# Kernel optimization log

Measured on AMD Instinct MI355X. Metric: run time of the kernel, lower is better.

The kernel has to match this reference:

```python
import jax, jax.numpy as jnp
import numpy as np

N = 100000      # nodes
E = 1600000     # edges
D_IN, H1, H2, D_OUT = 128, 64, 64, 64


def setup_inputs() -> dict:
    key = jax.random.key(0)
    ks = jax.random.split(key, 9)
    x = jax.random.normal(ks[0], (N, D_IN), dtype=jnp.float32)
    edge_index = jax.random.randint(ks[1], (2, E), 0, N, dtype=jnp.int32)
    def lin(k, fan_in, fan_out):
        s = 1.0 / np.sqrt(fan_in)
        return jax.random.uniform(k, (fan_in, fan_out), jnp.float32, -s, s)
    W1 = lin(ks[2], D_IN, H1); b1 = jnp.zeros((H1,), jnp.float32)
    W2 = lin(ks[3], H1, H2);  b2 = jnp.zeros((H2,), jnp.float32)
    W3 = lin(ks[4], H2, D_OUT); b3 = jnp.zeros((D_OUT,), jnp.float32)
    return {"x": x, "W1": W1, "b1": b1, "W2": W2, "b2": b2,
            "W3": W3, "b3": b3, "edge_index": edge_index}


def reference(x, W1, b1, W2, b2, W3, b3, edge_index):
    src, dst = edge_index[0], edge_index[1]
    # GCN symmetric normalization with self-loops: deg = in-degree + 1
    deg = jnp.zeros((N,), x.dtype).at[dst].add(1.0) + 1.0
    dinv = jax.lax.rsqrt(deg)                 # [N]
    norm = dinv[src] * dinv[dst]              # [E] edge weights
    self_norm = dinv * dinv                   # [N] self-loop weights

    def conv(h, W, b):
        h = h @ W                             # transform first (PyG GCNConv)
        msg = h[src] * norm[:, None]          # [E, F] gathered messages
        agg = jnp.zeros_like(h).at[dst].add(msg) + self_norm[:, None] * h
        return agg + b

    h = jax.nn.relu(conv(x, W1, b1))          # dropout is identity in eval
    h = jax.nn.relu(conv(h, W2, b2))
    return conv(h, W3, b3)
```

## Files before the change

kernel.cpp:

```cpp
#include <hip/hip_runtime.h>
#include <hip/hip_bf16.h>

#define D_IN 128
#define F 64
#define R_EDGES 4096

__global__ __launch_bounds__(256) void part1_kernel(
        const int* __restrict__ src, const int* __restrict__ dst, int E,
        unsigned long long M37, int cap1, uint2* __restrict__ ebufB,
        int* __restrict__ bcur1) {
    __shared__ int wcnt[64], incl64[64], cur[64], gbase[16];
    const int t = threadIdx.x, w = t >> 6, lane = t & 63;
    const int base = blockIdx.x * R_EDGES;
    const int lim = min(base + R_EDGES, E);

    if (t < 64) wcnt[t] = 0;
    __syncthreads();

    for (int i = base + t; i < lim; i += 256) {
        int d = dst[i];
        int b = (int)(((unsigned long long)(unsigned)d * M37) >> 37) >> 4;
        atomicAdd(&wcnt[b * 4 + w], 1);
    }
    __syncthreads();

    if (t < 64) {
        int v = wcnt[t], x = v;
        for (int dlt = 1; dlt < 64; dlt <<= 1) { int y = __shfl_up(x, dlt); if (lane >= dlt) x += y; }
        incl64[t] = x;
        wcnt[t] = x - v;
    }
    __syncthreads();
    if (t < 16) {
        int T = incl64[t * 4 + 3] - (t ? incl64[t * 4 - 1] : 0);
        gbase[t] = T > 0 ? atomicAdd(&bcur1[t], T) : 0;
    }
    __syncthreads();
    if (t < 64) cur[t] = gbase[t >> 2] + wcnt[t] - wcnt[(t >> 2) << 2];
    __syncthreads();

    for (int i = base + t; i < lim; i += 256) {
        int s = src[i], d = dst[i];
        int b = (int)(((unsigned long long)(unsigned)d * M37) >> 37) >> 4;
        int p = atomicAdd(&cur[b * 4 + w], 1);
        ebufB[(size_t)b * cap1 + p] = make_uint2((unsigned)s, (unsigned)d);
    }
}

#define BPB2 27
__global__ __launch_bounds__(256) void part2_kernel(
        const uint2* __restrict__ ebufB, const int* __restrict__ bcur1,
        unsigned long long M37, int cap1, int cap2,
        uint2* __restrict__ ebufA, int* __restrict__ bcur2) {
    __shared__ int wcnt[64], incl64[64], cur[64], gbase[16];
    const int t = threadIdx.x, w = t >> 6, lane = t & 63;
    const int b1 = blockIdx.x / BPB2, r = blockIdx.x % BPB2;
    const int cnt1 = bcur1[b1];
    const int beg = r * R_EDGES, lim = min(beg + R_EDGES, cnt1);
    if (beg >= cnt1) return;
    const uint2* in = ebufB + (size_t)b1 * cap1;

    if (t < 64) wcnt[t] = 0;
    __syncthreads();

    for (int i = beg + t; i < lim; i += 256) {
        unsigned d = in[i].y;
        int b = (int)(((unsigned long long)d * M37) >> 37) & 15;
        atomicAdd(&wcnt[b * 4 + w], 1);
    }
    __syncthreads();

    if (t < 64) {
        int v = wcnt[t], x = v;
        for (int dlt = 1; dlt < 64; dlt <<= 1) { int y = __shfl_up(x, dlt); if (lane >= dlt) x += y; }
        incl64[t] = x;
        wcnt[t] = x - v;
    }
    __syncthreads();
    if (t < 16) {
        int T = incl64[t * 4 + 3] - (t ? incl64[t * 4 - 1] : 0);
        gbase[t] = T > 0 ? atomicAdd(&bcur2[b1 * 16 + t], T) : 0;
    }
    __syncthreads();
    if (t < 64) cur[t] = gbase[t >> 2] + wcnt[t] - wcnt[(t >> 2) << 2];
    __syncthreads();

    for (int i = beg + t; i < lim; i += 256) {
        uint2 e = in[i];
        int b = (int)(((unsigned long long)e.y * M37) >> 37) & 15;
        int p = atomicAdd(&cur[b * 4 + w], 1);
        ebufA[(size_t)(b1 * 16 + b) * cap2 + p] = e;
    }
}

__global__ __launch_bounds__(256) void scan256_kernel(const int* __restrict__ bcur2,
                                                      int* __restrict__ bbase,
                                                      int* __restrict__ offsets, int n, int E) {
    __shared__ int tmp[256];
    int t = threadIdx.x;
    int v = bcur2[t];
    tmp[t] = v;
    __syncthreads();
    for (int off = 1; off < 256; off <<= 1) {
        int a = (t >= off) ? tmp[t - off] : 0;
        __syncthreads();
        if (t >= off) tmp[t] += a;
        __syncthreads();
    }
    bbase[t] = tmp[t] - v;
    if (t == 0) offsets[n] = E;
}

__global__ __launch_bounds__(256) void bsort_kernel(
        const uint2* __restrict__ ebufA, const int* __restrict__ bcur2,
        const int* __restrict__ bbase, int cap2, int NPB, int n,
        int* __restrict__ csr, int* __restrict__ offsets, float* __restrict__ dinv) {
    __shared__ int cnt[512], excl[512];
    const int sb = blockIdx.x, t = threadIdx.x;
    const int node0 = sb * NPB;
    const int nn = min(NPB, n - node0);
    if (nn <= 0) return;
    const int cE = bcur2[sb];
    const int base = bbase[sb];
    const uint2* eb = ebufA + (size_t)sb * cap2;

    for (int i = t; i < 512; i += 256) cnt[i] = 0;
    __syncthreads();
    for (int i = t; i < cE; i += 256) atomicAdd(&cnt[eb[i].y - node0], 1);
    __syncthreads();

    if (t < 64) {
        int carry = 0;
        for (int c = 0; c < 8; ++c) {
            int v = cnt[c * 64 + t], x = v;
            for (int dlt = 1; dlt < 64; dlt <<= 1) { int y = __shfl_up(x, dlt); if (t >= dlt) x += y; }
            excl[c * 64 + t] = carry + x - v;
            carry += __shfl(x, 63);
        }
    }
    __syncthreads();

    for (int i = t; i < nn; i += 256) {
        offsets[node0 + i] = base + excl[i];
        dinv[node0 + i] = rsqrtf((float)cnt[i] + 1.0f);
    }
    __syncthreads();
    for (int i = t; i < 512; i += 256) cnt[i] = excl[i];
    __syncthreads();
    for (int i = t; i < cE; i += 256) {
        uint2 e = eb[i];
        int p = atomicAdd(&cnt[e.y - node0], 1);
        csr[base + p] = (int)e.x;
    }
}

template<int K, bool RELU_IN>
__global__ __launch_bounds__(256) void gemm_kernel(
        const float* __restrict__ A, const float* __restrict__ W,
        const float* __restrict__ dinv, float* __restrict__ h2, int n) {
    constexpr int F4 = K / 4;
    __shared__ float4 Al[64 * F4];
    __shared__ float  Wl[K * F];
    const int t = threadIdx.x;

    for (int i = t; i < K * F / 4; i += 256)
        ((float4*)Wl)[i] = ((const float4*)W)[i];

    const int row0 = blockIdx.x * 64;
    for (int i = t; i < 64 * F4; i += 256) {
        int r = i / F4, k4 = i % F4;
        int gr = row0 + r; if (gr >= n) gr = n - 1;
        float4 v = ((const float4*)(A + (size_t)gr * K))[k4];
        if (RELU_IN) {
            v.x = fmaxf(v.x, 0.f); v.y = fmaxf(v.y, 0.f);
            v.z = fmaxf(v.z, 0.f); v.w = fmaxf(v.w, 0.f);
        }
        Al[r * F4 + (k4 ^ ((r >> 2) & 7))] = v;
    }
    __syncthreads();

    const int rg = t >> 4, cg = t & 15;
    const int r0 = rg * 4, c0 = cg * 4;
    const int sw = rg & 7;

    float acc[4][4] = {};
#pragma unroll 2
    for (int k4 = 0; k4 < F4; ++k4) {
        float4 a[4];
#pragma unroll
        for (int i = 0; i < 4; ++i) a[i] = Al[(r0 + i) * F4 + (k4 ^ sw)];
#pragma unroll
        for (int j = 0; j < 4; ++j) {
            float4 w = *(const float4*)&Wl[(k4 * 4 + j) * F + c0];
#pragma unroll
            for (int i = 0; i < 4; ++i) {
                float av = (j == 0) ? a[i].x : (j == 1) ? a[i].y : (j == 2) ? a[i].z : a[i].w;
                acc[i][0] = fmaf(av, w.x, acc[i][0]);
                acc[i][1] = fmaf(av, w.y, acc[i][1]);
                acc[i][2] = fmaf(av, w.z, acc[i][2]);
                acc[i][3] = fmaf(av, w.w, acc[i][3]);
            }
        }
    }

#pragma unroll
    for (int i = 0; i < 4; ++i) {
        int gr = row0 + r0 + i;
        if (gr < n) {
            float dv = dinv[gr];
            float4 o = make_float4(acc[i][0] * dv, acc[i][1] * dv,
                                   acc[i][2] * dv, acc[i][3] * dv);
            *(float4*)&h2[(size_t)gr * F + c0] = o;
        }
    }
}

__global__ __launch_bounds__(256) void agg_kernel(
        const int* __restrict__ offsets, const int* __restrict__ csr,
        const float* __restrict__ dinv, const float* __restrict__ h2,
        const float* __restrict__ bvec, float* __restrict__ out, int n) {
    const int wid  = (int)((blockIdx.x * 256u + threadIdx.x) >> 6);
    const int lane = threadIdx.x & 63;
    const int g = lane >> 4, q = lane & 15;
    if (wid >= n) return;

    const int beg = offsets[wid], end = offsets[wid + 1];

    float4 acc = make_float4(0.f, 0.f, 0.f, 0.f);
    if (g == 0) acc = *(const float4*)&h2[(size_t)wid * F + q * 4];

    int j = beg + g;
    for (; j + 4 < end; j += 8) {
        int s0 = csr[j], s1 = csr[j + 4];
        float4 v0 = *(const float4*)&h2[(size_t)s0 * F + q * 4];
        float4 v1 = *(const float4*)&h2[(size_t)s1 * F + q * 4];
        acc.x += v0.x + v1.x; acc.y += v0.y + v1.y;
        acc.z += v0.z + v1.z; acc.w += v0.w + v1.w;
    }
    if (j < end) {
        int s0 = csr[j];
        float4 v0 = *(const float4*)&h2[(size_t)s0 * F + q * 4];
        acc.x += v0.x; acc.y += v0.y; acc.z += v0.z; acc.w += v0.w;
    }

    acc.x += __shfl_xor(acc.x, 16); acc.y += __shfl_xor(acc.y, 16);
    acc.z += __shfl_xor(acc.z, 16); acc.w += __shfl_xor(acc.w, 16);
    acc.x += __shfl_xor(acc.x, 32); acc.y += __shfl_xor(acc.y, 32);
    acc.z += __shfl_xor(acc.z, 32); acc.w += __shfl_xor(acc.w, 32);

    if (g == 0) {
        float dv = dinv[wid];
        float4 bb = *(const float4*)&bvec[q * 4];
        float4 o = make_float4(fmaf(dv, acc.x, bb.x), fmaf(dv, acc.y, bb.y),
                               fmaf(dv, acc.z, bb.z), fmaf(dv, acc.w, bb.w));
        *(float4*)&out[(size_t)wid * F + q * 4] = o;
    }
}

extern "C" void kernel_launch(void* const* d_in, const int* in_sizes, int n_in,
                              void* d_out, int out_size, void* d_ws, size_t ws_size,
                              hipStream_t stream) {
    const float* x   = (const float*)d_in[0];
    const float* W1  = (const float*)d_in[1];
    const float* b1  = (const float*)d_in[2];
    const float* W2  = (const float*)d_in[3];
    const float* b2  = (const float*)d_in[4];
    const float* W3  = (const float*)d_in[5];
    const float* b3  = (const float*)d_in[6];
    const int*   ei  = (const int*)d_in[7];

    const int n = in_sizes[0] / D_IN;
    const int E = in_sizes[7] / 2;
    const int* src = ei;
    const int* dst = ei + E;

    const int NPB = (n + 255) >> 8;
    const unsigned long long M37 = ((1ull << 37) / (unsigned long long)NPB) + 1;
    const int cap1 = E / 16 + 4096;
    const int cap2 = 8192;

    char* p = (char*)d_ws;
    auto alloc = [&](size_t bytes) { char* q = p; p += (bytes + 255) & ~(size_t)255; return q; };
    int*   bcur1   = (int*)  alloc((16 + 256) * 4);
    int*   bcur2   = bcur1 + 16;
    int*   bbase   = (int*)  alloc(256 * 4);
    int*   offsets = (int*)  alloc((size_t)(n + 1) * 4);
    float* dinv    = (float*)alloc((size_t)n * 4);
    int*   csr     = (int*)  alloc((size_t)E * 4);
    float* h2      = (float*)alloc((size_t)n * F * 4);
    float* outA    = (float*)alloc((size_t)n * F * 4);
    float* outF    = (float*)d_out;

    uint2* ebufB = (uint2*)h2;
    uint2* ebufA = (uint2*)outA;

    const int p1Blocks = (E + R_EDGES - 1) / R_EDGES;
    const int gBlocks  = (n + 63) / 64;
    const int aBlocks  = (int)(((size_t)n * 64 + 255) / 256);

    hipMemsetAsync(bcur1, 0, (16 + 256) * 4, stream);
    part1_kernel <<<p1Blocks,  256, 0, stream>>>(src, dst, E, M37, cap1, ebufB, bcur1);
    part2_kernel <<<16 * BPB2, 256, 0, stream>>>(ebufB, bcur1, M37, cap1, cap2, ebufA, bcur2);
    scan256_kernel<<<1,        256, 0, stream>>>(bcur2, bbase, offsets, n, E);
    bsort_kernel <<<256,       256, 0, stream>>>(ebufA, bcur2, bbase, cap2, NPB, n,
                                                 csr, offsets, dinv);

    gemm_kernel<D_IN, false><<<gBlocks, 256, 0, stream>>>(x, W1, dinv, h2, n);
    agg_kernel<<<aBlocks, 256, 0, stream>>>(offsets, csr, dinv, h2, b1, outA, n);

    gemm_kernel<F, true><<<gBlocks, 256, 0, stream>>>(outA, W2, dinv, h2, n);
    agg_kernel<<<aBlocks, 256, 0, stream>>>(offsets, csr, dinv, h2, b2, outA, n);

    gemm_kernel<F, true><<<gBlocks, 256, 0, stream>>>(outA, W3, dinv, h2, n);
    agg_kernel<<<aBlocks, 256, 0, stream>>>(offsets, csr, dinv, h2, b3, outF, n);
}
```

Before: 314.9 us.

## Fuse aggregation with next layer's GEMM and unroll neighbor gathers by four

Adds an aggmm kernel that aggregates 64 nodes per block (bias plus ReLU), keeps the results in swizzled shared memory, and immediately multiplies them by the next layer's weights. This removes two GEMM launches and the write and re-read of the intermediate activations. The agg loop is also unrolled to four gathers in flight per lane group. The risk is lower parallelism: one wave now handles 16 nodes in sequence, so fewer waves are available to hide gather latency.

```diff
diff --git a/kernel.cpp b/kernel.cpp
--- a/kernel.cpp
+++ b/kernel.cpp
@@ -215,6 +215,101 @@
     }
 }
 
+__global__ __launch_bounds__(256) void aggmm_kernel(
+        const int* __restrict__ offsets, const int* __restrict__ csr,
+        const float* __restrict__ dinv, const float* __restrict__ hin,
+        const float* __restrict__ bvec, const float* __restrict__ W,
+        float* __restrict__ hout, int n) {
+    __shared__ float4 Al[64 * 16];
+    __shared__ float  Wl[64 * F];
+    const int t = threadIdx.x;
+
+    for (int i = t; i < 64 * F / 4; i += 256)
+        ((float4*)Wl)[i] = ((const float4*)W)[i];
+
+    const int row0 = blockIdx.x * 64;
+    const int wv = t >> 6, lane = t & 63;
+    const int g = lane >> 4, q = lane & 15;
+
+    for (int i = 0; i < 16; ++i) {
+        const int r = wv * 16 + i;
+        const int node = row0 + r;
+        if (node < n) {
+            float4 acc = make_float4(0.f, 0.f, 0.f, 0.f);
+            if (g == 0) acc = *(const float4*)&hin[(size_t)node * F + q * 4];
+            const int beg = offsets[node], end = offsets[node + 1];
+            int j = beg + g;
+            for (; j + 12 < end; j += 16) {
+                int s0 = csr[j], s1 = csr[j + 4], s2 = csr[j + 8], s3 = csr[j + 12];
+                float4 v0 = *(const float4*)&hin[(size_t)s0 * F + q * 4];
+                float4 v1 = *(const float4*)&hin[(size_t)s1 * F + q * 4];
+                float4 v2 = *(const float4*)&hin[(size_t)s2 * F + q * 4];
+                float4 v3 = *(const float4*)&hin[(size_t)s3 * F + q * 4];
+                acc.x += (v0.x + v1.x) + (v2.x + v3.x);
+                acc.y += (v0.y + v1.y) + (v2.y + v3.y);
+                acc.z += (v0.z + v1.z) + (v2.z + v3.z);
+                acc.w += (v0.w + v1.w) + (v2.w + v3.w);
+            }
+            for (; j < end; j += 4) {
+                int s0 = csr[j];
+                float4 v0 = *(const float4*)&hin[(size_t)s0 * F + q * 4];
+                acc.x += v0.x; acc.y += v0.y; acc.z += v0.z; acc.w += v0.w;
+            }
+            acc.x += __shfl_xor(acc.x, 16); acc.y += __shfl_xor(acc.y, 16);
+            acc.z += __shfl_xor(acc.z, 16); acc.w += __shfl_xor(acc.w, 16);
+            acc.x += __shfl_xor(acc.x, 32); acc.y += __shfl_xor(acc.y, 32);
+            acc.z += __shfl_xor(acc.z, 32); acc.w += __shfl_xor(acc.w, 32);
+            if (g == 0) {
+                float dv = dinv[node];
+                float4 bb = *(const float4*)&bvec[q * 4];
+                float4 o = make_float4(fmaxf(fmaf(dv, acc.x, bb.x), 0.f),
+                                       fmaxf(fmaf(dv, acc.y, bb.y), 0.f),
+                                       fmaxf(fmaf(dv, acc.z, bb.z), 0.f),
+                                       fmaxf(fmaf(dv, acc.w, bb.w), 0.f));
+                Al[r * 16 + (q ^ ((r >> 2) & 7))] = o;
+            }
+        } else if (g == 0) {
+            Al[r * 16 + (q ^ ((r >> 2) & 7))] = make_float4(0.f, 0.f, 0.f, 0.f);
+        }
+    }
+    __syncthreads();
+
+    const int rg = t >> 4, cg = t & 15;
+    const int r0 = rg * 4, c0 = cg * 4;
+    const int sw = rg & 7;
+
+    float acc[4][4] = {};
+#pragma unroll 2
+    for (int k4 = 0; k4 < 16; ++k4) {
+        float4 a[4];
+#pragma unroll
+        for (int i = 0; i < 4; ++i) a[i] = Al[(r0 + i) * 16 + (k4 ^ sw)];
+#pragma unroll
+        for (int j = 0; j < 4; ++j) {
+            float4 w = *(const float4*)&Wl[(k4 * 4 + j) * F + c0];
+#pragma unroll
+            for (int i = 0; i < 4; ++i) {
+                float av = (j == 0) ? a[i].x : (j == 1) ? a[i].y : (j == 2) ? a[i].z : a[i].w;
+                acc[i][0] = fmaf(av, w.x, acc[i][0]);
+                acc[i][1] = fmaf(av, w.y, acc[i][1]);
+                acc[i][2] = fmaf(av, w.z, acc[i][2]);
+                acc[i][3] = fmaf(av, w.w, acc[i][3]);
+            }
+        }
+    }
+
+#pragma unroll
+    for (int i = 0; i < 4; ++i) {
+        int gr = row0 + r0 + i;
+        if (gr < n) {
+            float dv = dinv[gr];
+            float4 o = make_float4(acc[i][0] * dv, acc[i][1] * dv,
+                                   acc[i][2] * dv, acc[i][3] * dv);
+            *(float4*)&hout[(size_t)gr * F + c0] = o;
+        }
+    }
+}
+
 __global__ __launch_bounds__(256) void agg_kernel(
         const int* __restrict__ offsets, const int* __restrict__ csr,
         const float* __restrict__ dinv, const float* __restrict__ h2,
@@ -230,14 +325,18 @@
     if (g == 0) acc = *(const float4*)&h2[(size_t)wid * F + q * 4];
 
     int j = beg + g;
-    for (; j + 4 < end; j += 8) {
-        int s0 = csr[j], s1 = csr[j + 4];
+    for (; j + 12 < end; j += 16) {
+        int s0 = csr[j], s1 = csr[j + 4], s2 = csr[j + 8], s3 = csr[j + 12];
         float4 v0 = *(const float4*)&h2[(size_t)s0 * F + q * 4];
         float4 v1 = *(const float4*)&h2[(size_t)s1 * F + q * 4];
-        acc.x += v0.x + v1.x; acc.y += v0.y + v1.y;
-        acc.z += v0.z + v1.z; acc.w += v0.w + v1.w;
-    }
-    if (j < end) {
+        float4 v2 = *(const float4*)&h2[(size_t)s2 * F + q * 4];
+        float4 v3 = *(const float4*)&h2[(size_t)s3 * F + q * 4];
+        acc.x += (v0.x + v1.x) + (v2.x + v3.x);
+        acc.y += (v0.y + v1.y) + (v2.y + v3.y);
+        acc.z += (v0.z + v1.z) + (v2.z + v3.z);
+        acc.w += (v0.w + v1.w) + (v2.w + v3.w);
+    }
+    for (; j < end; j += 4) {
         int s0 = csr[j];
         float4 v0 = *(const float4*)&h2[(size_t)s0 * F + q * 4];
         acc.x += v0.x; acc.y += v0.y; acc.z += v0.z; acc.w += v0.w;
@@ -287,12 +386,12 @@
     int*   offsets = (int*)  alloc((size_t)(n + 1) * 4);
     float* dinv    = (float*)alloc((size_t)n * 4);
     int*   csr     = (int*)  alloc((size_t)E * 4);
-    float* h2      = (float*)alloc((size_t)n * F * 4);
-    float* outA    = (float*)alloc((size_t)n * F * 4);
+    float* hA      = (float*)alloc((size_t)n * F * 4);
+    float* hB      = (float*)alloc((size_t)n * F * 4);
     float* outF    = (float*)d_out;
 
-    uint2* ebufB = (uint2*)h2;
-    uint2* ebufA = (uint2*)outA;
+    uint2* ebufB = (uint2*)hA;
+    uint2* ebufA = (uint2*)hB;
 
     const int p1Blocks = (E + R_EDGES - 1) / R_EDGES;
     const int gBlocks  = (n + 63) / 64;
@@ -305,12 +404,8 @@
     bsort_kernel <<<256,       256, 0, stream>>>(ebufA, bcur2, bbase, cap2, NPB, n,
                                                  csr, offsets, dinv);
 
-    gemm_kernel<D_IN, false><<<gBlocks, 256, 0, stream>>>(x, W1, dinv, h2, n);
-    agg_kernel<<<aBlocks, 256, 0, stream>>>(offsets, csr, dinv, h2, b1, outA, n);
-
-    gemm_kernel<F, true><<<gBlocks, 256, 0, stream>>>(outA, W2, dinv, h2, n);
-    agg_kernel<<<aBlocks, 256, 0, stream>>>(offsets, csr, dinv, h2, b2, outA, n);
-
-    gemm_kernel<F, true><<<gBlocks, 256, 0, stream>>>(outA, W3, dinv, h2, n);
-    agg_kernel<<<aBlocks, 256, 0, stream>>>(offsets, csr, dinv, h2, b3, outF, n);
-}
+    gemm_kernel<D_IN, false><<<gBlocks, 256, 0, stream>>>(x, W1, dinv, hA, n);
+    aggmm_kernel<<<gBlocks, 256, 0, stream>>>(offsets, csr, dinv, hA, b1, W2, hB, n);
+    aggmm_kernel<<<gBlocks, 256, 0, stream>>>(offsets, csr, dinv, hB, b2, W3, hA, n);
+    agg_kernel<<<aBlocks, 256, 0, stream>>>(offsets, csr, dinv, hA, b3, outF, n);
+}
```

Result: slower. 374.3 us (+18.9%).
